# Performance work log

Measured on AMD Instinct MI355X. Metric: run time of the kernel, lower is better.

Reference implementation:

```python
import jax, jax.numpy as jnp
import numpy as np

N_NODES = 100000
N_EDGES = 3200000
D_IN = 256
D_OUT = 256


def setup_inputs() -> dict:
    key = jax.random.key(0)
    k1, k2, k3, k4, k5 = jax.random.split(key, 5)
    x = jax.random.normal(k1, (N_NODES, D_IN), dtype=jnp.float32)
    W = jax.random.normal(k2, (D_OUT, D_IN), dtype=jnp.float32) * (1.0 / np.sqrt(D_IN))
    edge_val = jax.random.uniform(k3, (N_EDGES,), dtype=jnp.float32)
    edge_row = jax.random.randint(k4, (N_EDGES,), 0, N_NODES, dtype=jnp.int32)
    edge_col = jax.random.randint(k5, (N_EDGES,), 0, N_NODES, dtype=jnp.int32)
    return {"x": x, "W": W, "edge_val": edge_val, "edge_row": edge_row, "edge_col": edge_col}


def reference(x, W, edge_val, edge_row, edge_col):
    # Linear (no bias): [N, D_in] @ [D_in, D_out] -> [N, D_out]
    h = x @ W.T
    # SpMM: out[r] = sum_e val[e] * h[col[e]] for edges with row[e] == r
    msgs = h[edge_col] * edge_val[:, None]          # [E, D_out] gather + scale
    out = jax.ops.segment_sum(msgs, edge_row, num_segments=N_NODES)  # scatter-add
    return out
```

## Files before the change

kernel.cpp:

```cpp
#include <hip/hip_runtime.h>
#include <hip/hip_bf16.h>

typedef float  f32x4 __attribute__((ext_vector_type(4)));
typedef short  s16x8 __attribute__((ext_vector_type(8)));
typedef unsigned short u16x8 __attribute__((ext_vector_type(8)));

#define N_NODES 100000
#define N_EDGES 3200000
#define DD 256

#define ROWS_PER_BKT 128
#define NBKT 782
#define BKT_CAP 4608
#define ACHUNK 3072
#define NABLK 1042
#define EDGES_PER_THREAD 12

#define GEMM_BLOCKS 1563

__device__ __forceinline__ ushort f2bf(float f) {
    union { __hip_bfloat16 b; ushort u; } cv;
    cv.b = __float2bfloat16(f);
    return cv.u;
}

__global__ __launch_bounds__(256) void wconv_kernel(const float* __restrict__ w, ushort* __restrict__ wb)
{
    int gid = blockIdx.x * 256 + threadIdx.x;
    float4 a = ((const float4*)w)[gid * 2];
    float4 b = ((const float4*)w)[gid * 2 + 1];
    u16x8 o = { f2bf(a.x), f2bf(a.y), f2bf(a.z), f2bf(a.w),
                f2bf(b.x), f2bf(b.y), f2bf(b.z), f2bf(b.w) };
    ((u16x8*)wb)[gid] = o;
}

__global__ __launch_bounds__(256) void gemm_q_kernel(
    const float* __restrict__ x, const ushort* __restrict__ wb,
    unsigned char* __restrict__ h8, float* __restrict__ hscale)
{
    __shared__ float wmax[64 * 4];
    const int tid  = threadIdx.x;
    const int lane = tid & 63;
    const int wq   = tid >> 6;
    const int bm   = blockIdx.x * 64;
    const int l15  = lane & 15;
    const int lhi  = lane >> 4;
    f32x4 acc[4][4] = {};

    bool rowok[4];
    #pragma unroll
    for (int m = 0; m < 4; ++m) rowok[m] = (bm + m * 16 + l15) < N_NODES;

    const float*  xbase = x  + (size_t)(bm + l15) * DD + lhi * 8;
    const ushort* wbase = wb + (size_t)(wq * 64 + l15) * DD + lhi * 8;

    #pragma unroll 2
    for (int kk = 0; kk < 8; ++kk) {
        s16x8 a[4], b[4];
        #pragma unroll
        for (int n = 0; n < 4; ++n)
            b[n] = *(const s16x8*)(wbase + (size_t)(n * 16) * DD + kk * 32);
        #pragma unroll
        for (int m = 0; m < 4; ++m) {
            float4 lo = make_float4(0.f, 0.f, 0.f, 0.f);
            float4 hi = make_float4(0.f, 0.f, 0.f, 0.f);
            if (rowok[m]) {
                const float* p = xbase + (size_t)(m * 16) * DD + kk * 32;
                lo = *(const float4*)p;
                hi = *(const float4*)(p + 4);
            }
            a[m] = (s16x8){ (short)f2bf(lo.x), (short)f2bf(lo.y), (short)f2bf(lo.z), (short)f2bf(lo.w),
                            (short)f2bf(hi.x), (short)f2bf(hi.y), (short)f2bf(hi.z), (short)f2bf(hi.w) };
        }
        #pragma unroll
        for (int m = 0; m < 4; ++m)
            #pragma unroll
            for (int n = 0; n < 4; ++n)
                acc[m][n] = __builtin_amdgcn_mfma_f32_16x16x32_bf16(a[m], b[n], acc[m][n], 0, 0, 0);
    }

    float pmax[4][4];
    #pragma unroll
    for (int m = 0; m < 4; ++m)
        #pragma unroll
        for (int r = 0; r < 4; ++r)
            pmax[m][r] = fmaxf(fmaxf(fabsf(acc[m][0][r]), fabsf(acc[m][1][r])),
                               fmaxf(fabsf(acc[m][2][r]), fabsf(acc[m][3][r])));
    #pragma unroll
    for (int s = 1; s < 16; s <<= 1)
        #pragma unroll
        for (int m = 0; m < 4; ++m)
            #pragma unroll
            for (int r = 0; r < 4; ++r)
                pmax[m][r] = fmaxf(pmax[m][r], __shfl_xor(pmax[m][r], s));
    if (l15 == 0) {
        #pragma unroll
        for (int m = 0; m < 4; ++m)
            #pragma unroll
            for (int r = 0; r < 4; ++r)
                wmax[(m * 16 + lhi * 4 + r) * 4 + wq] = pmax[m][r];
    }
    __syncthreads();
    #pragma unroll
    for (int m = 0; m < 4; ++m)
        #pragma unroll
        for (int r = 0; r < 4; ++r) {
            const int R = m * 16 + lhi * 4 + r;
            const int row = bm + R;
            if (row >= N_NODES) continue;
            f32x4 wv = *(const f32x4*)&wmax[R * 4];
            float rmax = fmaxf(fmaxf(fmaxf(wv[0], wv[1]), fmaxf(wv[2], wv[3])), 1e-30f);
            const float sc = 127.0f * __builtin_amdgcn_rcpf(rmax);
            int q0 = (int)rintf(acc[m][0][r] * sc);
            int q1 = (int)rintf(acc[m][1][r] * sc);
            int q2 = (int)rintf(acc[m][2][r] * sc);
            int q3 = (int)rintf(acc[m][3][r] * sc);
            unsigned pack = (q0 & 255) | ((q1 & 255) << 8) | ((q2 & 255) << 16) | ((unsigned)(q3 & 255) << 24);
            *(unsigned*)(h8 + (size_t)row * DD + wq * 64 + l15 * 4) = pack;
            if (wq == 0 && l15 == 0) hscale[row] = rmax * (1.0f / 127.0f);
        }
}

__global__ __launch_bounds__(256) void passA_kernel(
    const int* __restrict__ erow, const int* __restrict__ ecol,
    const float* __restrict__ eval, int* __restrict__ gcur,
    int2* __restrict__ pairsA)
{
    __shared__ int hist[NBKT];
    __shared__ int sbase[NBKT];
    __shared__ int scur[NBKT];
    __shared__ int rbase[NBKT];
    __shared__ int gsum[256];
    __shared__ int2 staged[ACHUNK];
    __shared__ int gdst[ACHUNK];
    const int tid = threadIdx.x;
    for (int i = tid; i < NBKT; i += 256) hist[i] = 0;
    __syncthreads();
    const int base = blockIdx.x * ACHUNK;
    int pk[EDGES_PER_THREAD]; float vv[EDGES_PER_THREAD]; int bk[EDGES_PER_THREAD];
    #pragma unroll
    for (int k = 0; k < EDGES_PER_THREAD; ++k) {
        int i = base + k * 256 + tid;
        bk[k] = -1;
        if (i < N_EDGES) {
            int r = erow[i];
            bk[k] = r >> 7;
            pk[k] = ecol[i] | ((r & 127) << 17);
            vv[k] = eval[i];
            atomicAdd(&hist[bk[k]], 1);
        }
    }
    __syncthreads();
    int gs = 0, lv[4];
    #pragma unroll
    for (int j = 0; j < 4; ++j) {
        int b = tid * 4 + j;
        lv[j] = (b < NBKT) ? hist[b] : 0;
        gs += lv[j];
    }
    gsum[tid] = gs;
    __syncthreads();
    for (int s = 1; s < 256; s <<= 1) {
        int t = (tid >= s) ? gsum[tid - s] : 0;
        __syncthreads();
        gsum[tid] += t;
        __syncthreads();
    }
    int run = gsum[tid] - gs;
    #pragma unroll
    for (int j = 0; j < 4; ++j) {
        int b = tid * 4 + j;
        if (b < NBKT) { sbase[b] = run; scur[b] = run; }
        run += lv[j];
    }
    __syncthreads();
    for (int b = tid; b < NBKT; b += 256) {
        int c = hist[b];
        if (c) rbase[b] = atomicAdd(&gcur[b], c);
    }
    __syncthreads();
    #pragma unroll
    for (int k = 0; k < EDGES_PER_THREAD; ++k) {
        if (bk[k] >= 0) {
            int lo = atomicAdd(&scur[bk[k]], 1);
            staged[lo] = make_int2(pk[k], __float_as_int(vv[k]));
            gdst[lo] = bk[k] * BKT_CAP + rbase[bk[k]] + (lo - sbase[bk[k]]);
        }
    }
    __syncthreads();
    const int cnt = min(ACHUNK, N_EDGES - base);
    for (int t = tid; t < cnt; t += 256)
        pairsA[gdst[t]] = staged[t];
}

__global__ __launch_bounds__(256) void passB_kernel(
    const int2* __restrict__ pairsA, const int* __restrict__ gcur,
    int2* __restrict__ pairsB, int2* __restrict__ row_se)
{
    __shared__ int hist[ROWS_PER_BKT];
    __shared__ int lds[ROWS_PER_BKT];
    __shared__ int cur[ROWS_PER_BKT];
    const int tid = threadIdx.x;
    const int b = blockIdx.x;
    const int cnt = gcur[b];
    const int base = b * BKT_CAP;
    if (tid < ROWS_PER_BKT) hist[tid] = 0;
    __syncthreads();
    for (int i = tid; i < cnt; i += 256)
        atomicAdd(&hist[(pairsA[base + i].x >> 17) & 127], 1);
    __syncthreads();
    int v = (tid < ROWS_PER_BKT) ? hist[tid] : 0;
    if (tid < ROWS_PER_BKT) lds[tid] = v;
    __syncthreads();
    for (int st = 1; st < ROWS_PER_BKT; st <<= 1) {
        int t = (tid >= st && tid < ROWS_PER_BKT) ? lds[tid - st] : 0;
        __syncthreads();
        if (tid < ROWS_PER_BKT) lds[tid] += t;
        __syncthreads();
    }
    if (tid < ROWS_PER_BKT) {
        int excl = lds[tid] - v;
        int r = b * ROWS_PER_BKT + tid;
        if (r < N_NODES) row_se[r] = make_int2(base + excl, base + excl + v);
        cur[tid] = base + excl;
    }
    __syncthreads();
    for (int i = tid; i < cnt; i += 256) {
        int2 p = pairsA[base + i];
        int rl = (p.x >> 17) & 127;
        int d = atomicAdd(&cur[rl], 1);
        pairsB[d] = make_int2(p.x & 0x1FFFF, p.y);
    }
}

__global__ __launch_bounds__(256) void spmm_kernel(
    const unsigned char* __restrict__ h8, const float* __restrict__ hscale,
    const int2* __restrict__ pairs, const int2* __restrict__ row_se,
    float* __restrict__ out)
{
    __shared__ float obuf[4][256];
    const int wave = threadIdx.x >> 6;
    const int wid  = blockIdx.x * 4 + wave;
    const int lane = threadIdx.x & 63;
    if (wid >= N_NODES) return;
    const int2 se = row_se[wid];
    const int s = __builtin_amdgcn_readfirstlane(se.x);
    const int e = __builtin_amdgcn_readfirstlane(se.y);
    const int loff = lane * 4;
    const int colbase = (lane >> 4) * 64 + (lane & 15);
    float ax = 0.f, ay = 0.f, az = 0.f, aw = 0.f;

    int j = s;
    for (; j + 8 <= e; j += 8) {
        const int4* p4 = (const int4*)(pairs + j);
        int4 q0 = p4[0], q1 = p4[1], q2 = p4[2], q3 = p4[3];
        int   c[8] = { q0.x, q0.z, q1.x, q1.z, q2.x, q2.z, q3.x, q3.z };
        float v[8] = { __int_as_float(q0.y), __int_as_float(q0.w),
                       __int_as_float(q1.y), __int_as_float(q1.w),
                       __int_as_float(q2.y), __int_as_float(q2.w),
                       __int_as_float(q3.y), __int_as_float(q3.w) };
        float vs[8];
        #pragma unroll
        for (int t = 0; t < 8; ++t) vs[t] = v[t] * hscale[c[t]];
        unsigned hv[8];
        #pragma unroll
        for (int t = 0; t < 8; ++t)
            hv[t] = *(const unsigned*)(h8 + (size_t)c[t] * DD + loff);
        #pragma unroll
        for (int t = 0; t < 8; ++t) {
            ax += vs[t] * (float)((int)(hv[t] << 24) >> 24);
            ay += vs[t] * (float)((int)(hv[t] << 16) >> 24);
            az += vs[t] * (float)((int)(hv[t] <<  8) >> 24);
            aw += vs[t] * (float)((int)hv[t] >> 24);
        }
    }
    for (; j < e; ++j) {
        int2 p = pairs[j];
        const float vs = __int_as_float(p.y) * hscale[p.x];
        const unsigned hv = *(const unsigned*)(h8 + (size_t)p.x * DD + loff);
        ax += vs * (float)((int)(hv << 24) >> 24);
        ay += vs * (float)((int)(hv << 16) >> 24);
        az += vs * (float)((int)(hv <<  8) >> 24);
        aw += vs * (float)((int)hv >> 24);
    }
    obuf[wave][colbase +  0] = ax;
    obuf[wave][colbase + 16] = ay;
    obuf[wave][colbase + 32] = az;
    obuf[wave][colbase + 48] = aw;
    f32x4 o = *(const f32x4*)&obuf[wave][loff];
    __builtin_nontemporal_store(o, (f32x4*)(out + (size_t)wid * DD + loff));
}

extern "C" void kernel_launch(void* const* d_in, const int* in_sizes, int n_in,
                              void* d_out, int out_size, void* d_ws, size_t ws_size,
                              hipStream_t stream)
{
    const float* x        = (const float*)d_in[0];
    const float* W        = (const float*)d_in[1];
    const float* edge_val = (const float*)d_in[2];
    const int*   edge_row = (const int*)d_in[3];
    const int*   edge_col = (const int*)d_in[4];
    float* out = (float*)d_out;

    char* ws = (char*)d_ws;
    size_t off = 0;
    auto alloc = [&](size_t bytes) {
        void* p = ws + off;
        off = (off + bytes + 255) & ~(size_t)255;
        return p;
    };
    unsigned char* h8     = (unsigned char*)alloc((size_t)N_NODES * DD);
    float*         hscale = (float*)alloc((size_t)N_NODES * sizeof(float));
    int2*          pairsA = (int2*)alloc((size_t)NBKT * BKT_CAP * sizeof(int2));
    int2*          pairsB = (int2*)alloc((size_t)NBKT * BKT_CAP * sizeof(int2));
    ushort*        wb     = (ushort*)alloc((size_t)DD * DD * sizeof(ushort));
    int*           gcur   = (int*)alloc((size_t)NBKT * sizeof(int));
    int2*          row_se = (int2*)alloc((size_t)N_NODES * sizeof(int2));
    (void)ws_size;

    (void)hipMemsetAsync(gcur, 0, (size_t)NBKT * sizeof(int), stream);

    wconv_kernel<<<DD * DD / 8 / 256, 256, 0, stream>>>(W, wb);

    gemm_q_kernel<<<GEMM_BLOCKS, 256, 0, stream>>>(x, wb, h8, hscale);

    passA_kernel<<<NABLK, 256, 0, stream>>>(edge_row, edge_col, edge_val, gcur, pairsA);

    passB_kernel<<<NBKT, 256, 0, stream>>>(pairsA, gcur, pairsB, row_se);

    int spmm_blocks = (N_NODES + 3) / 4;
    spmm_kernel<<<spmm_blocks, 256, 0, stream>>>(h8, hscale, pairsB, row_se, out);
}
```

Measured before the change: 293.4 us.

## Merge GEMM-quantize and edge bucketing pass into one launch, stage x in LDS

Combines the bf16 GEMM+int8 quantization kernel and the edge bucketing pass A into a single launch whose block index selects the role, so the two independent workloads can run concurrently and one launch boundary disappears. The GEMM path now loads the 64-row x tile coalesced into padded LDS as bf16 before the MFMA loop, instead of each lane loading strided fp32 directly. Shared memory becomes dynamic and sized for the larger pass-A layout, which may reduce occupancy for the GEMM blocks.

```diff
diff --git a/kernel.cpp b/kernel.cpp
--- a/kernel.cpp
+++ b/kernel.cpp
@@ -17,6 +17,9 @@
 #define EDGES_PER_THREAD 12
 
 #define GEMM_BLOCKS 1563
+#define XLDP 264
+
+#define K1_LDS (4*NBKT*4 + 256*4 + ACHUNK*8 + ACHUNK*4)
 
 __device__ __forceinline__ ushort f2bf(float f) {
     union { __hip_bfloat16 b; ushort u; } cv;
@@ -34,109 +37,108 @@
     ((u16x8*)wb)[gid] = o;
 }
 
-__global__ __launch_bounds__(256) void gemm_q_kernel(
+__global__ __launch_bounds__(256) void k1_kernel(
     const float* __restrict__ x, const ushort* __restrict__ wb,
-    unsigned char* __restrict__ h8, float* __restrict__ hscale)
-{
-    __shared__ float wmax[64 * 4];
-    const int tid  = threadIdx.x;
-    const int lane = tid & 63;
-    const int wq   = tid >> 6;
-    const int bm   = blockIdx.x * 64;
-    const int l15  = lane & 15;
-    const int lhi  = lane >> 4;
-    f32x4 acc[4][4] = {};
-
-    bool rowok[4];
-    #pragma unroll
-    for (int m = 0; m < 4; ++m) rowok[m] = (bm + m * 16 + l15) < N_NODES;
-
-    const float*  xbase = x  + (size_t)(bm + l15) * DD + lhi * 8;
-    const ushort* wbase = wb + (size_t)(wq * 64 + l15) * DD + lhi * 8;
-
-    #pragma unroll 2
-    for (int kk = 0; kk < 8; ++kk) {
-        s16x8 a[4], b[4];
-        #pragma unroll
-        for (int n = 0; n < 4; ++n)
-            b[n] = *(const s16x8*)(wbase + (size_t)(n * 16) * DD + kk * 32);
-        #pragma unroll
-        for (int m = 0; m < 4; ++m) {
-            float4 lo = make_float4(0.f, 0.f, 0.f, 0.f);
-            float4 hi = make_float4(0.f, 0.f, 0.f, 0.f);
-            if (rowok[m]) {
-                const float* p = xbase + (size_t)(m * 16) * DD + kk * 32;
-                lo = *(const float4*)p;
-                hi = *(const float4*)(p + 4);
-            }
-            a[m] = (s16x8){ (short)f2bf(lo.x), (short)f2bf(lo.y), (short)f2bf(lo.z), (short)f2bf(lo.w),
-                            (short)f2bf(hi.x), (short)f2bf(hi.y), (short)f2bf(hi.z), (short)f2bf(hi.w) };
-        }
-        #pragma unroll
-        for (int m = 0; m < 4; ++m)
-            #pragma unroll
-            for (int n = 0; n < 4; ++n)
-                acc[m][n] = __builtin_amdgcn_mfma_f32_16x16x32_bf16(a[m], b[n], acc[m][n], 0, 0, 0);
-    }
-
-    float pmax[4][4];
-    #pragma unroll
-    for (int m = 0; m < 4; ++m)
-        #pragma unroll
-        for (int r = 0; r < 4; ++r)
-            pmax[m][r] = fmaxf(fmaxf(fabsf(acc[m][0][r]), fabsf(acc[m][1][r])),
-                               fmaxf(fabsf(acc[m][2][r]), fabsf(acc[m][3][r])));
-    #pragma unroll
-    for (int s = 1; s < 16; s <<= 1)
-        #pragma unroll
-        for (int m = 0; m < 4; ++m)
-            #pragma unroll
-            for (int r = 0; r < 4; ++r)
-                pmax[m][r] = fmaxf(pmax[m][r], __shfl_xor(pmax[m][r], s));
-    if (l15 == 0) {
-        #pragma unroll
-        for (int m = 0; m < 4; ++m)
-            #pragma unroll
-            for (int r = 0; r < 4; ++r)
-                wmax[(m * 16 + lhi * 4 + r) * 4 + wq] = pmax[m][r];
-    }
-    __syncthreads();
-    #pragma unroll
-    for (int m = 0; m < 4; ++m)
-        #pragma unroll
-        for (int r = 0; r < 4; ++r) {
-            const int R = m * 16 + lhi * 4 + r;
-            const int row = bm + R;
-            if (row >= N_NODES) continue;
-            f32x4 wv = *(const f32x4*)&wmax[R * 4];
-            float rmax = fmaxf(fmaxf(fmaxf(wv[0], wv[1]), fmaxf(wv[2], wv[3])), 1e-30f);
-            const float sc = 127.0f * __builtin_amdgcn_rcpf(rmax);
-            int q0 = (int)rintf(acc[m][0][r] * sc);
-            int q1 = (int)rintf(acc[m][1][r] * sc);
-            int q2 = (int)rintf(acc[m][2][r] * sc);
-            int q3 = (int)rintf(acc[m][3][r] * sc);
-            unsigned pack = (q0 & 255) | ((q1 & 255) << 8) | ((q2 & 255) << 16) | ((unsigned)(q3 & 255) << 24);
-            *(unsigned*)(h8 + (size_t)row * DD + wq * 64 + l15 * 4) = pack;
-            if (wq == 0 && l15 == 0) hscale[row] = rmax * (1.0f / 127.0f);
-        }
-}
-
-__global__ __launch_bounds__(256) void passA_kernel(
+    unsigned char* __restrict__ h8, float* __restrict__ hscale,
     const int* __restrict__ erow, const int* __restrict__ ecol,
     const float* __restrict__ eval, int* __restrict__ gcur,
     int2* __restrict__ pairsA)
 {
-    __shared__ int hist[NBKT];
-    __shared__ int sbase[NBKT];
-    __shared__ int scur[NBKT];
-    __shared__ int rbase[NBKT];
-    __shared__ int gsum[256];
-    __shared__ int2 staged[ACHUNK];
-    __shared__ int gdst[ACHUNK];
+    extern __shared__ char smem[];
     const int tid = threadIdx.x;
+
+    if (blockIdx.x < GEMM_BLOCKS) {
+        ushort (*xs)[XLDP] = (ushort(*)[XLDP])smem;
+        const int lane = tid & 63;
+        const int wq   = tid >> 6;
+        const int bm   = blockIdx.x * 64;
+        const int l15  = lane & 15;
+        const int lhi  = lane >> 4;
+
+        #pragma unroll
+        for (int it = 0; it < 16; ++it) {
+            int f = (it * 256 + tid) * 4;
+            int r = f >> 8, c = f & 255;
+            float4 v = make_float4(0.f, 0.f, 0.f, 0.f);
+            if (bm + r < N_NODES) v = *(const float4*)(x + (size_t)(bm + r) * DD + c);
+            *(ushort4*)&xs[r][c] = make_ushort4(f2bf(v.x), f2bf(v.y), f2bf(v.z), f2bf(v.w));
+        }
+        __syncthreads();
+
+        f32x4 acc[4][4] = {};
+        const ushort* wbase = wb + (size_t)(wq * 64 + l15) * DD + lhi * 8;
+        #pragma unroll 2
+        for (int kk = 0; kk < 8; ++kk) {
+            s16x8 a[4], b[4];
+            #pragma unroll
+            for (int n = 0; n < 4; ++n)
+                b[n] = *(const s16x8*)(wbase + (size_t)(n * 16) * DD + kk * 32);
+            #pragma unroll
+            for (int m = 0; m < 4; ++m)
+                a[m] = *(const s16x8*)&xs[m * 16 + l15][kk * 32 + lhi * 8];
+            #pragma unroll
+            for (int m = 0; m < 4; ++m)
+                #pragma unroll
+                for (int n = 0; n < 4; ++n)
+                    acc[m][n] = __builtin_amdgcn_mfma_f32_16x16x32_bf16(a[m], b[n], acc[m][n], 0, 0, 0);
+        }
+
+        __syncthreads();
+        float* wmax = (float*)smem;
+        float pmax[4][4];
+        #pragma unroll
+        for (int m = 0; m < 4; ++m)
+            #pragma unroll
+            for (int r = 0; r < 4; ++r)
+                pmax[m][r] = fmaxf(fmaxf(fabsf(acc[m][0][r]), fabsf(acc[m][1][r])),
+                                   fmaxf(fabsf(acc[m][2][r]), fabsf(acc[m][3][r])));
+        #pragma unroll
+        for (int s = 1; s < 16; s <<= 1)
+            #pragma unroll
+            for (int m = 0; m < 4; ++m)
+                #pragma unroll
+                for (int r = 0; r < 4; ++r)
+                    pmax[m][r] = fmaxf(pmax[m][r], __shfl_xor(pmax[m][r], s));
+        if (l15 == 0) {
+            #pragma unroll
+            for (int m = 0; m < 4; ++m)
+                #pragma unroll
+                for (int r = 0; r < 4; ++r)
+                    wmax[(m * 16 + lhi * 4 + r) * 4 + wq] = pmax[m][r];
+        }
+        __syncthreads();
+        #pragma unroll
+        for (int m = 0; m < 4; ++m)
+            #pragma unroll
+            for (int r = 0; r < 4; ++r) {
+                const int R = m * 16 + lhi * 4 + r;
+                const int row = bm + R;
+                if (row >= N_NODES) continue;
+                f32x4 wv = *(const f32x4*)&wmax[R * 4];
+                float rmax = fmaxf(fmaxf(fmaxf(wv[0], wv[1]), fmaxf(wv[2], wv[3])), 1e-30f);
+                const float sc = 127.0f * __builtin_amdgcn_rcpf(rmax);
+                int q0 = (int)rintf(acc[m][0][r] * sc);
+                int q1 = (int)rintf(acc[m][1][r] * sc);
+                int q2 = (int)rintf(acc[m][2][r] * sc);
+                int q3 = (int)rintf(acc[m][3][r] * sc);
+                unsigned pack = (q0 & 255) | ((q1 & 255) << 8) | ((q2 & 255) << 16) | ((unsigned)(q3 & 255) << 24);
+                *(unsigned*)(h8 + (size_t)row * DD + wq * 64 + l15 * 4) = pack;
+                if (wq == 0 && l15 == 0) hscale[row] = rmax * (1.0f / 127.0f);
+            }
+        return;
+    }
+
+    int*  hist   = (int*)smem;
+    int*  sbase  = hist  + NBKT;
+    int*  scur   = sbase + NBKT;
+    int*  rbase  = scur  + NBKT;
+    int*  gsum   = rbase + NBKT;
+    int2* staged = (int2*)(gsum + 256);
+    int*  gdst   = (int*)(staged + ACHUNK);
+
     for (int i = tid; i < NBKT; i += 256) hist[i] = 0;
     __syncthreads();
-    const int base = blockIdx.x * ACHUNK;
+    const int base = (blockIdx.x - GEMM_BLOCKS) * ACHUNK;
     int pk[EDGES_PER_THREAD]; float vv[EDGES_PER_THREAD]; int bk[EDGES_PER_THREAD];
     #pragma unroll
     for (int k = 0; k < EDGES_PER_THREAD; ++k) {
@@ -322,9 +324,8 @@
 
     wconv_kernel<<<DD * DD / 8 / 256, 256, 0, stream>>>(W, wb);
 
-    gemm_q_kernel<<<GEMM_BLOCKS, 256, 0, stream>>>(x, wb, h8, hscale);
-
-    passA_kernel<<<NABLK, 256, 0, stream>>>(edge_row, edge_col, edge_val, gcur, pairsA);
+    k1_kernel<<<GEMM_BLOCKS + NABLK, 256, K1_LDS, stream>>>(
+        x, wb, h8, hscale, edge_row, edge_col, edge_val, gcur, pairsA);
 
     passB_kernel<<<NBKT, 256, 0, stream>>>(pairsA, gcur, pairsB, row_se);
 
```

New measurement: 241.0 us, median of 2. -17.9%, faster.

## Stage x tile in LDS as bf16 in GEMM and pad bucket counters

Applied to the files above, without the earlier changes.

The GEMM kernel now loads each 64-row x tile once with coalesced float4 reads, converts it to bf16 into a padded shared-memory buffer, and feeds MFMA A operands from LDS. Before, each of the four waves separately re-read and re-converted the same x rows from global memory. Separately, the per-bucket atomic counters are spaced 16 ints apart so contended atomics land on different cache lines. The changes add LDS usage (about 33KB per block), which may reduce occupancy, plus an extra barrier. The padded counters enlarge the memset slightly.

```diff
diff --git a/kernel.cpp b/kernel.cpp
--- a/kernel.cpp
+++ b/kernel.cpp
@@ -15,8 +15,10 @@
 #define ACHUNK 3072
 #define NABLK 1042
 #define EDGES_PER_THREAD 12
+#define GSTRIDE 16
 
 #define GEMM_BLOCKS 1563
+#define XLDP 264
 
 __device__ __forceinline__ ushort f2bf(float f) {
     union { __hip_bfloat16 b; ushort u; } cv;
@@ -38,22 +40,26 @@
     const float* __restrict__ x, const ushort* __restrict__ wb,
     unsigned char* __restrict__ h8, float* __restrict__ hscale)
 {
-    __shared__ float wmax[64 * 4];
+    __shared__ ushort xs[64][XLDP];
     const int tid  = threadIdx.x;
     const int lane = tid & 63;
     const int wq   = tid >> 6;
     const int bm   = blockIdx.x * 64;
     const int l15  = lane & 15;
     const int lhi  = lane >> 4;
+
+    #pragma unroll
+    for (int it = 0; it < 16; ++it) {
+        int f = (it * 256 + tid) * 4;
+        int r = f >> 8, c = f & 255;
+        float4 v = make_float4(0.f, 0.f, 0.f, 0.f);
+        if (bm + r < N_NODES) v = *(const float4*)(x + (size_t)(bm + r) * DD + c);
+        *(ushort4*)&xs[r][c] = make_ushort4(f2bf(v.x), f2bf(v.y), f2bf(v.z), f2bf(v.w));
+    }
+    __syncthreads();
+
     f32x4 acc[4][4] = {};
-
-    bool rowok[4];
-    #pragma unroll
-    for (int m = 0; m < 4; ++m) rowok[m] = (bm + m * 16 + l15) < N_NODES;
-
-    const float*  xbase = x  + (size_t)(bm + l15) * DD + lhi * 8;
     const ushort* wbase = wb + (size_t)(wq * 64 + l15) * DD + lhi * 8;
-
     #pragma unroll 2
     for (int kk = 0; kk < 8; ++kk) {
         s16x8 a[4], b[4];
@@ -61,17 +67,8 @@
         for (int n = 0; n < 4; ++n)
             b[n] = *(const s16x8*)(wbase + (size_t)(n * 16) * DD + kk * 32);
         #pragma unroll
-        for (int m = 0; m < 4; ++m) {
-            float4 lo = make_float4(0.f, 0.f, 0.f, 0.f);
-            float4 hi = make_float4(0.f, 0.f, 0.f, 0.f);
-            if (rowok[m]) {
-                const float* p = xbase + (size_t)(m * 16) * DD + kk * 32;
-                lo = *(const float4*)p;
-                hi = *(const float4*)(p + 4);
-            }
-            a[m] = (s16x8){ (short)f2bf(lo.x), (short)f2bf(lo.y), (short)f2bf(lo.z), (short)f2bf(lo.w),
-                            (short)f2bf(hi.x), (short)f2bf(hi.y), (short)f2bf(hi.z), (short)f2bf(hi.w) };
-        }
+        for (int m = 0; m < 4; ++m)
+            a[m] = *(const s16x8*)&xs[m * 16 + l15][kk * 32 + lhi * 8];
         #pragma unroll
         for (int m = 0; m < 4; ++m)
             #pragma unroll
@@ -79,6 +76,8 @@
                 acc[m][n] = __builtin_amdgcn_mfma_f32_16x16x32_bf16(a[m], b[n], acc[m][n], 0, 0, 0);
     }
 
+    __syncthreads();
+    float* wmax = (float*)&xs[0][0];
     float pmax[4][4];
     #pragma unroll
     for (int m = 0; m < 4; ++m)
@@ -176,7 +175,7 @@
     __syncthreads();
     for (int b = tid; b < NBKT; b += 256) {
         int c = hist[b];
-        if (c) rbase[b] = atomicAdd(&gcur[b], c);
+        if (c) rbase[b] = atomicAdd(&gcur[b * GSTRIDE], c);
     }
     __syncthreads();
     #pragma unroll
@@ -202,7 +201,7 @@
     __shared__ int cur[ROWS_PER_BKT];
     const int tid = threadIdx.x;
     const int b = blockIdx.x;
-    const int cnt = gcur[b];
+    const int cnt = gcur[b * GSTRIDE];
     const int base = b * BKT_CAP;
     if (tid < ROWS_PER_BKT) hist[tid] = 0;
     __syncthreads();
@@ -314,11 +313,11 @@
     int2*          pairsA = (int2*)alloc((size_t)NBKT * BKT_CAP * sizeof(int2));
     int2*          pairsB = (int2*)alloc((size_t)NBKT * BKT_CAP * sizeof(int2));
     ushort*        wb     = (ushort*)alloc((size_t)DD * DD * sizeof(ushort));
-    int*           gcur   = (int*)alloc((size_t)NBKT * sizeof(int));
+    int*           gcur   = (int*)alloc((size_t)NBKT * GSTRIDE * sizeof(int));
     int2*          row_se = (int2*)alloc((size_t)N_NODES * sizeof(int2));
     (void)ws_size;
 
-    (void)hipMemsetAsync(gcur, 0, (size_t)NBKT * sizeof(int), stream);
+    (void)hipMemsetAsync(gcur, 0, (size_t)NBKT * GSTRIDE * sizeof(int), stream);
 
     wconv_kernel<<<DD * DD / 8 / 256, 256, 0, stream>>>(W, wb);
 
```

New measurement: 288.0 us. No clear change (-1.9%).
